# Kernel tuning notes

Hardware: AMD Instinct MI355X
Metric: run time of the kernel (lower is better)

## Reference

```python
import jax, jax.numpy as jnp
import numpy as np

D = 1024
H = 16
HD = D // H


def setup_inputs() -> dict:
    key = jax.random.key(0)
    k1, k2, k3 = jax.random.split(key, 3)
    x = jax.random.normal(k1, (4, 2048, D), dtype=jnp.float32)
    # torch Linear weight is [out, in]; we store transposed [in, out] for x @ W
    w_qkv = jax.random.normal(k2, (D, 3 * D), dtype=jnp.float32) * (1.0 / np.sqrt(D))
    w_o = jax.random.normal(k3, (D, D), dtype=jnp.float32) * (1.0 / np.sqrt(D))
    return {"x": x, "w_qkv": w_qkv, "w_o": w_o}


def reference(x, w_qkv, w_o):
    B, T, _ = x.shape
    qkv = x @ w_qkv                                  # [B, T, 3D]
    q, k, v = jnp.split(qkv, 3, axis=-1)
    def heads(t):
        return t.reshape(B, T, H, HD).transpose(0, 2, 1, 3)  # [B, H, T, hd]
    q, k, v = heads(q), heads(k), heads(v)
    scale = 1.0 / jnp.sqrt(jnp.asarray(HD, x.dtype))
    att = jnp.einsum("bhtd,bhsd->bhts", q, k) * scale       # [B, H, T, T]
    att = jax.nn.softmax(att, axis=-1)
    y = jnp.einsum("bhts,bhsd->bhtd", att, v)                # [B, H, T, hd]
    y = y.transpose(0, 2, 1, 3).reshape(B, T, D)
    return y @ w_o
```

## Files before the change

### kernel.cpp

```cpp
#include <hip/hip_runtime.h>
#include <hip/hip_bf16.h>
#include <stdint.h>

typedef __attribute__((ext_vector_type(8))) short short8;
typedef __attribute__((ext_vector_type(4))) float f32x4;

#define MFMA_BF16(a, b, c) __builtin_amdgcn_mfma_f32_16x16x32_bf16((a), (b), (c), 0, 0, 0)

#define QSCALE 0.18033688011118293f

__device__ __forceinline__ unsigned short f2bf(float f) {
  unsigned int u = __builtin_bit_cast(unsigned int, f);
  u += 0x7fffu + ((u >> 16) & 1u);
  return (unsigned short)(u >> 16);
}

__device__ __forceinline__ uint32_t pkbf(float a, float b) {
  float2 f; f.x = a; f.y = b;
  __hip_bfloat162 h = __float22bfloat162_rn(f);
  uint32_t u;
  __builtin_memcpy(&u, &h, 4);
  return u;
}

__device__ __forceinline__ float exp2_fast(float x) {
#if __has_builtin(__builtin_amdgcn_exp2f)
  return __builtin_amdgcn_exp2f(x);
#else
  float r;
  asm("v_exp_f32 %0, %1" : "=v"(r) : "v"(x));
  return r;
#endif
}

__device__ __forceinline__ void gload_lds16(const void* g, void* l) {
  __builtin_amdgcn_global_load_lds(
      (const __attribute__((address_space(1))) unsigned int*)g,
      (__attribute__((address_space(3))) unsigned int*)l, 16, 0, 0);
}

__global__ __launch_bounds__(256) void cvt_f32_bf16_k(const float* __restrict__ in,
                                                      unsigned short* __restrict__ out,
                                                      int n8) {
  int i = blockIdx.x * 256 + threadIdx.x;
  if (i >= n8) return;
  const float4* p = (const float4*)(in + (size_t)i * 8);
  float4 a = p[0], b = p[1];
  short8 o;
  o[0] = (short)f2bf(a.x); o[1] = (short)f2bf(a.y);
  o[2] = (short)f2bf(a.z); o[3] = (short)f2bf(a.w);
  o[4] = (short)f2bf(b.x); o[5] = (short)f2bf(b.y);
  o[6] = (short)f2bf(b.z); o[7] = (short)f2bf(b.w);
  *(short8*)(out + (size_t)i * 8) = o;
}

__global__ __launch_bounds__(256) void transpose_f32_bf16_k(const float* __restrict__ in,
                                                            unsigned short* __restrict__ out,
                                                            int R, int C) {
  __shared__ __attribute__((aligned(16))) unsigned short t[64][65];
  int c0 = blockIdx.x * 64, r0 = blockIdx.y * 64;
  int tx = threadIdx.x;
  for (int rr = threadIdx.y; rr < 64; rr += 4)
    t[rr][tx] = f2bf(in[(size_t)(r0 + rr) * C + c0 + tx]);
  __syncthreads();
  for (int rr = threadIdx.y; rr < 64; rr += 4)
    out[(size_t)(c0 + rr) * R + r0 + tx] = t[tx][rr];
}

template <int MODE, int NT>
__global__ __launch_bounds__(256, 3) void gemm_bt_k(
    const unsigned short* __restrict__ A, const unsigned short* __restrict__ Bt,
    float* __restrict__ Cout, unsigned short* __restrict__ Qd,
    unsigned short* __restrict__ Kd, unsigned short* __restrict__ Vtd,
    int M, int N, int Kdim) {
  __shared__ __attribute__((aligned(16))) unsigned short As[3][4096];
  __shared__ __attribute__((aligned(16))) unsigned short Bs[3][4096];
  const int tid = threadIdx.x, lane = tid & 63, w = tid >> 6;
  const int wr = w >> 1, wc = w & 1;
  const int lo = lane & 15, hi = lane >> 4;
  const int nwg = gridDim.x;
  const int newid = (blockIdx.x & 7) * (nwg >> 3) + (blockIdx.x >> 3);
  const int tn = newid % NT, tm = newid / NT;
  f32x4 acc[4][4] = {};
  const char* Ab = (const char*)A;
  const char* Bb = (const char*)Bt;
  const int nk = Kdim >> 5;

#define GSTAGE(kt, bb)                                                        \
  {                                                                           \
    _Pragma("unroll") for (int j = 0; j < 2; ++j) {                           \
      int o8 = w * 2048 + j * 1024 + lane * 16;                               \
      int src = o8 ^ (((o8 >> 6) & 3) << 4);                                  \
      int row = src >> 6, cb = src & 63;                                      \
      gload_lds16(Ab + ((size_t)(tm * 128 + row) * Kdim + (kt) * 32) * 2 + cb,\
                  (char*)As[bb] + o8);                                        \
      gload_lds16(Bb + ((size_t)(tn * 128 + row) * Kdim + (kt) * 32) * 2 + cb,\
                  (char*)Bs[bb] + o8);                                        \
    }                                                                         \
  }

  GSTAGE(0, 0);
  GSTAGE(1, 1);
  asm volatile("s_waitcnt vmcnt(4)" ::: "memory");
  __builtin_amdgcn_s_barrier();
  int gbuf = 0;
  for (int kt = 0; kt < nk; ++kt) {
    if (kt + 2 < nk) {
      int nb = gbuf + 2; if (nb >= 3) nb -= 3;
      GSTAGE(kt + 2, nb);
    }
    short8 af[4], bf[4];
#pragma unroll
    for (int m = 0; m < 4; ++m) {
      int r = wr * 64 + m * 16 + lo;
      int ad = (r * 64 + hi * 16) ^ ((r & 3) << 4);
      af[m] = *(const short8*)((const char*)As[gbuf] + ad);
    }
#pragma unroll
    for (int n = 0; n < 4; ++n) {
      int r = wc * 64 + n * 16 + lo;
      int ad = (r * 64 + hi * 16) ^ ((r & 3) << 4);
      bf[n] = *(const short8*)((const char*)Bs[gbuf] + ad);
    }
    __builtin_amdgcn_s_setprio(1);
#pragma unroll
    for (int m = 0; m < 4; ++m)
#pragma unroll
      for (int n = 0; n < 4; ++n)
        acc[m][n] = MFMA_BF16(af[m], bf[n], acc[m][n]);
    __builtin_amdgcn_s_setprio(0);
    if (kt + 2 < nk)
      asm volatile("s_waitcnt vmcnt(4)" ::: "memory");
    else
      asm volatile("s_waitcnt vmcnt(0)" ::: "memory");
    __builtin_amdgcn_s_barrier();
    gbuf = (gbuf + 1 == 3) ? 0 : gbuf + 1;
  }
  if (MODE == 1) {
#pragma unroll
    for (int m = 0; m < 4; ++m)
#pragma unroll
      for (int n = 0; n < 4; ++n)
#pragma unroll
        for (int j = 0; j < 4; ++j) {
          int row = tm * 128 + wr * 64 + m * 16 + hi * 4 + j;
          int col = tn * 128 + wc * 64 + n * 16 + lo;
          Cout[(size_t)row * N + col] = acc[m][n][j];
        }
  } else {
    int which = (tn * 128) >> 10;
#pragma unroll
    for (int m = 0; m < 4; ++m)
#pragma unroll
      for (int n = 0; n < 4; ++n)
#pragma unroll
        for (int j = 0; j < 4; ++j) {
          int row = tm * 128 + wr * 64 + m * 16 + hi * 4 + j;
          int col = tn * 128 + wc * 64 + n * 16 + lo;
          int b = row >> 11, t = row & 2047;
          int rem = col & 1023;
          int h = rem >> 6, hd = rem & 63;
          float v = acc[m][n][j];
          if (which == 0)
            Qd[((size_t)(b * 16 + h) * 2048 + t) * 64 + hd] = f2bf(v * QSCALE);
          else if (which == 1)
            Kd[((size_t)(b * 16 + h) * 2048 + t) * 64 + hd] = f2bf(v);
          else
            Vtd[((size_t)(b * 16 + h) * 64 + hd) * 2048 + t] = f2bf(v);
        }
  }
}

__global__ __launch_bounds__(512) void attn_k(const unsigned short* __restrict__ Qd,
                                              const unsigned short* __restrict__ Kd,
                                              const unsigned short* __restrict__ Vtd,
                                              unsigned short* __restrict__ Y) {
  const int T = 2048, NT = 32;
  int flat = blockIdx.x;
  int qt = (flat >> 3) & 7;
  int bh = (flat & 7) * 8 + (flat >> 6);
  int tid = threadIdx.x, lane = tid & 63, w = tid >> 6;
  int lo = lane & 15, hi = lane >> 4;
  const unsigned short* Qbh = Qd + (size_t)bh * T * 64;
  const char* Kb = (const char*)(Kd + (size_t)bh * T * 64);
  const char* Vb = (const char*)(Vtd + (size_t)bh * 64 * T);

  __shared__ __attribute__((aligned(16))) unsigned short Ks[3][4096];
  __shared__ __attribute__((aligned(16))) unsigned short Vs[3][4096];
  __shared__ __attribute__((aligned(16))) unsigned short Ps[8][2][1024];

  const short8 ones = {0x3F80, 0x3F80, 0x3F80, 0x3F80,
                       0x3F80, 0x3F80, 0x3F80, 0x3F80};

  short8 qf[2][2];
#pragma unroll
  for (int qh = 0; qh < 2; ++qh) {
    const unsigned short* qrow =
        Qbh + (size_t)(qt * 256 + w * 32 + qh * 16 + lo) * 64 + hi * 8;
    qf[qh][0] = *(const short8*)qrow;
    qf[qh][1] = *(const short8*)(qrow + 32);
  }
  f32x4 oacc[2][4] = {};
  f32x4 lacc[2] = {};

#define STAGE(kt, b)                                                          \
  {                                                                           \
    int base = w * 1024;                                                      \
    int o8 = base + lane * 16;                                                \
    int src = o8 ^ (((o8 >> 7) & 7) << 4);                                    \
    gload_lds16(Kb + (size_t)(kt) * 8192 + src, (char*)Ks[b] + base);         \
    int hd_ = src >> 7, cbyt = src & 127;                                     \
    gload_lds16(Vb + (size_t)hd_ * (T * 2) + (size_t)(kt) * 128 + cbyt,       \
                (char*)Vs[b] + base);                                         \
  }

  STAGE(0, 0);
  STAGE(1, 1);
  asm volatile("s_waitcnt vmcnt(2)" ::: "memory");
  __builtin_amdgcn_s_barrier();
  int bufc = 0;
  for (int kt = 0; kt < NT; ++kt) {
    if (kt + 2 < NT) {
      int nb = bufc + 2; if (nb >= 3) nb -= 3;
      STAGE(kt + 2, nb);
    }

    f32x4 sacc[2][4] = {};
    __builtin_amdgcn_s_setprio(1);
#pragma unroll
    for (int st = 0; st < 4; ++st)
#pragma unroll
      for (int c = 0; c < 2; ++c) {
        int row = st * 16 + lo;
        int addr = (row * 128 + c * 64 + hi * 16) ^ ((row & 7) << 4);
        short8 kf = *(const short8*)((const char*)Ks[bufc] + addr);
        sacc[0][st] = MFMA_BF16(kf, qf[0][c], sacc[0][st]);
        sacc[1][st] = MFMA_BF16(kf, qf[1][c], sacc[1][st]);
      }
    __builtin_amdgcn_s_setprio(0);

#pragma unroll
    for (int qh = 0; qh < 2; ++qh) {
      char* pw = (char*)&Ps[w][qh][0];
#pragma unroll
      for (int st = 0; st < 4; ++st) {
        float p0 = exp2_fast(sacc[qh][st][0]);
        float p1 = exp2_fast(sacc[qh][st][1]);
        float p2 = exp2_fast(sacc[qh][st][2]);
        float p3 = exp2_fast(sacc[qh][st][3]);
        int wb = (lo * 128 + st * 32 + hi * 8) ^ ((lo & 7) << 4);
        *(uint32_t*)(pw + wb) = pkbf(p0, p1);
        *(uint32_t*)(pw + wb + 4) = pkbf(p2, p3);
      }
    }

    __builtin_amdgcn_s_setprio(1);
#pragma unroll
    for (int c = 0; c < 2; ++c) {
      int pb = (lo * 128 + c * 64 + hi * 16) ^ ((lo & 7) << 4);
      short8 pf0 = *(const short8*)((const char*)&Ps[w][0][0] + pb);
      short8 pf1 = *(const short8*)((const char*)&Ps[w][1][0] + pb);
      lacc[0] = MFMA_BF16(pf0, ones, lacc[0]);
      lacc[1] = MFMA_BF16(pf1, ones, lacc[1]);
#pragma unroll
      for (int n = 0; n < 4; ++n) {
        int row = n * 16 + lo;
        int addr = (row * 128 + c * 64 + hi * 16) ^ ((row & 7) << 4);
        short8 vf = *(const short8*)((const char*)Vs[bufc] + addr);
        oacc[0][n] = MFMA_BF16(pf0, vf, oacc[0][n]);
        oacc[1][n] = MFMA_BF16(pf1, vf, oacc[1][n]);
      }
    }
    __builtin_amdgcn_s_setprio(0);

    if (kt + 2 < NT)
      asm volatile("s_waitcnt vmcnt(2)" ::: "memory");
    else
      asm volatile("s_waitcnt vmcnt(0)" ::: "memory");
    __builtin_amdgcn_s_barrier();
    bufc = (bufc + 1 == 3) ? 0 : bufc + 1;
  }

  int b = bh >> 4, h = bh & 15;
#pragma unroll
  for (int qh = 0; qh < 2; ++qh)
#pragma unroll
    for (int r = 0; r < 4; ++r) {
      int t = qt * 256 + w * 32 + qh * 16 + hi * 4 + r;
      float rl = 1.0f / lacc[qh][r];
#pragma unroll
      for (int n = 0; n < 4; ++n) {
        int hd = n * 16 + lo;
        Y[((size_t)(b * 2048 + t)) * 1024 + h * 64 + hd] =
            f2bf(oacc[qh][n][r] * rl);
      }
    }
}

extern "C" void kernel_launch(void* const* d_in, const int* in_sizes, int n_in,
                              void* d_out, int out_size, void* d_ws, size_t ws_size,
                              hipStream_t stream) {
  const float* x = (const float*)d_in[0];
  const float* w_qkv = (const float*)d_in[1];
  const float* w_o = (const float*)d_in[2];
  float* out = (float*)d_out;
  char* ws = (char*)d_ws;
  unsigned short* xb    = (unsigned short*)(ws + 0);
  unsigned short* wqkvT = (unsigned short*)(ws + 16777216);
  unsigned short* woT   = (unsigned short*)(ws + 23068672);
  unsigned short* qb    = (unsigned short*)(ws + 25165824);
  unsigned short* kb    = (unsigned short*)(ws + 41943040);
  unsigned short* vtb   = (unsigned short*)(ws + 58720256);
  unsigned short* yb    = xb;

  cvt_f32_bf16_k<<<4096, 256, 0, stream>>>(x, xb, 1048576);
  transpose_f32_bf16_k<<<dim3(48, 16), dim3(64, 4), 0, stream>>>(w_qkv, wqkvT, 1024, 3072);
  transpose_f32_bf16_k<<<dim3(16, 16), dim3(64, 4), 0, stream>>>(w_o, woT, 1024, 1024);
  gemm_bt_k<0, 24><<<1536, 256, 0, stream>>>(xb, wqkvT, nullptr, qb, kb, vtb,
                                             8192, 3072, 1024);
  attn_k<<<512, 512, 0, stream>>>(qb, kb, vtb, yb);
  gemm_bt_k<1, 8><<<512, 256, 0, stream>>>(yb, woT, out, nullptr, nullptr, nullptr,
                                           8192, 1024, 1024);
}
```

Measured before the change: 215.7 us.

## Give each attention wave 64 query rows with 256-thread blocks

```diff
diff --git a/kernel.cpp b/kernel.cpp
--- a/kernel.cpp
+++ b/kernel.cpp
@@ -171,7 +171,7 @@
   }
 }
 
-__global__ __launch_bounds__(512) void attn_k(const unsigned short* __restrict__ Qd,
+__global__ __launch_bounds__(256) void attn_k(const unsigned short* __restrict__ Qd,
                                               const unsigned short* __restrict__ Kd,
                                               const unsigned short* __restrict__ Vtd,
                                               unsigned short* __restrict__ Y) {
@@ -187,36 +187,38 @@
 
   __shared__ __attribute__((aligned(16))) unsigned short Ks[3][4096];
   __shared__ __attribute__((aligned(16))) unsigned short Vs[3][4096];
-  __shared__ __attribute__((aligned(16))) unsigned short Ps[8][2][1024];
+  __shared__ __attribute__((aligned(16))) unsigned short Ps[4][4][1024];
 
   const short8 ones = {0x3F80, 0x3F80, 0x3F80, 0x3F80,
                        0x3F80, 0x3F80, 0x3F80, 0x3F80};
 
-  short8 qf[2][2];
-#pragma unroll
-  for (int qh = 0; qh < 2; ++qh) {
+  short8 qf[4][2];
+#pragma unroll
+  for (int qh = 0; qh < 4; ++qh) {
     const unsigned short* qrow =
-        Qbh + (size_t)(qt * 256 + w * 32 + qh * 16 + lo) * 64 + hi * 8;
+        Qbh + (size_t)(qt * 256 + w * 64 + qh * 16 + lo) * 64 + hi * 8;
     qf[qh][0] = *(const short8*)qrow;
     qf[qh][1] = *(const short8*)(qrow + 32);
   }
-  f32x4 oacc[2][4] = {};
-  f32x4 lacc[2] = {};
+  f32x4 oacc[4][4] = {};
+  f32x4 lacc[4] = {};
 
 #define STAGE(kt, b)                                                          \
   {                                                                           \
-    int base = w * 1024;                                                      \
-    int o8 = base + lane * 16;                                                \
-    int src = o8 ^ (((o8 >> 7) & 7) << 4);                                    \
-    gload_lds16(Kb + (size_t)(kt) * 8192 + src, (char*)Ks[b] + base);         \
-    int hd_ = src >> 7, cbyt = src & 127;                                     \
-    gload_lds16(Vb + (size_t)hd_ * (T * 2) + (size_t)(kt) * 128 + cbyt,       \
-                (char*)Vs[b] + base);                                         \
+    _Pragma("unroll") for (int j = 0; j < 2; ++j) {                           \
+      int dst = w * 2048 + j * 1024;                                          \
+      int o8 = dst + lane * 16;                                               \
+      int src = o8 ^ (((o8 >> 7) & 7) << 4);                                  \
+      gload_lds16(Kb + (size_t)(kt) * 8192 + src, (char*)Ks[b] + dst);        \
+      int hd_ = src >> 7, cbyt = src & 127;                                   \
+      gload_lds16(Vb + (size_t)hd_ * (T * 2) + (size_t)(kt) * 128 + cbyt,     \
+                  (char*)Vs[b] + dst);                                        \
+    }                                                                         \
   }
 
   STAGE(0, 0);
   STAGE(1, 1);
-  asm volatile("s_waitcnt vmcnt(2)" ::: "memory");
+  asm volatile("s_waitcnt vmcnt(4)" ::: "memory");
   __builtin_amdgcn_s_barrier();
   int bufc = 0;
   for (int kt = 0; kt < NT; ++kt) {
@@ -225,7 +227,7 @@
       STAGE(kt + 2, nb);
     }
 
-    f32x4 sacc[2][4] = {};
+    f32x4 sacc[4][4] = {};
     __builtin_amdgcn_s_setprio(1);
 #pragma unroll
     for (int st = 0; st < 4; ++st)
@@ -234,13 +236,14 @@
         int row = st * 16 + lo;
         int addr = (row * 128 + c * 64 + hi * 16) ^ ((row & 7) << 4);
         short8 kf = *(const short8*)((const char*)Ks[bufc] + addr);
-        sacc[0][st] = MFMA_BF16(kf, qf[0][c], sacc[0][st]);
-        sacc[1][st] = MFMA_BF16(kf, qf[1][c], sacc[1][st]);
+#pragma unroll
+        for (int qh = 0; qh < 4; ++qh)
+          sacc[qh][st] = MFMA_BF16(kf, qf[qh][c], sacc[qh][st]);
       }
     __builtin_amdgcn_s_setprio(0);
 
 #pragma unroll
-    for (int qh = 0; qh < 2; ++qh) {
+    for (int qh = 0; qh < 4; ++qh) {
       char* pw = (char*)&Ps[w][qh][0];
 #pragma unroll
       for (int st = 0; st < 4; ++st) {
@@ -249,8 +252,10 @@
         float p2 = exp2_fast(sacc[qh][st][2]);
         float p3 = exp2_fast(sacc[qh][st][3]);
         int wb = (lo * 128 + st * 32 + hi * 8) ^ ((lo & 7) << 4);
-        *(uint32_t*)(pw + wb) = pkbf(p0, p1);
-        *(uint32_t*)(pw + wb + 4) = pkbf(p2, p3);
+        uint2 pk;
+        pk.x = pkbf(p0, p1);
+        pk.y = pkbf(p2, p3);
+        *(uint2*)(pw + wb) = pk;
       }
     }
 
@@ -258,23 +263,26 @@
 #pragma unroll
     for (int c = 0; c < 2; ++c) {
       int pb = (lo * 128 + c * 64 + hi * 16) ^ ((lo & 7) << 4);
-      short8 pf0 = *(const short8*)((const char*)&Ps[w][0][0] + pb);
-      short8 pf1 = *(const short8*)((const char*)&Ps[w][1][0] + pb);
-      lacc[0] = MFMA_BF16(pf0, ones, lacc[0]);
-      lacc[1] = MFMA_BF16(pf1, ones, lacc[1]);
+      short8 pf[4];
+#pragma unroll
+      for (int qh = 0; qh < 4; ++qh) {
+        pf[qh] = *(const short8*)((const char*)&Ps[w][qh][0] + pb);
+        lacc[qh] = MFMA_BF16(pf[qh], ones, lacc[qh]);
+      }
 #pragma unroll
       for (int n = 0; n < 4; ++n) {
         int row = n * 16 + lo;
         int addr = (row * 128 + c * 64 + hi * 16) ^ ((row & 7) << 4);
         short8 vf = *(const short8*)((const char*)Vs[bufc] + addr);
-        oacc[0][n] = MFMA_BF16(pf0, vf, oacc[0][n]);
-        oacc[1][n] = MFMA_BF16(pf1, vf, oacc[1][n]);
+#pragma unroll
+        for (int qh = 0; qh < 4; ++qh)
+          oacc[qh][n] = MFMA_BF16(pf[qh], vf, oacc[qh][n]);
       }
     }
     __builtin_amdgcn_s_setprio(0);
 
     if (kt + 2 < NT)
-      asm volatile("s_waitcnt vmcnt(2)" ::: "memory");
+      asm volatile("s_waitcnt vmcnt(4)" ::: "memory");
     else
       asm volatile("s_waitcnt vmcnt(0)" ::: "memory");
     __builtin_amdgcn_s_barrier();
@@ -283,10 +291,10 @@
 
   int b = bh >> 4, h = bh & 15;
 #pragma unroll
-  for (int qh = 0; qh < 2; ++qh)
+  for (int qh = 0; qh < 4; ++qh)
 #pragma unroll
     for (int r = 0; r < 4; ++r) {
-      int t = qt * 256 + w * 32 + qh * 16 + hi * 4 + r;
+      int t = qt * 256 + w * 64 + qh * 16 + hi * 4 + r;
       float rl = 1.0f / lacc[qh][r];
 #pragma unroll
       for (int n = 0; n < 4; ++n) {
@@ -318,7 +326,7 @@
   transpose_f32_bf16_k<<<dim3(16, 16), dim3(64, 4), 0, stream>>>(w_o, woT, 1024, 1024);
   gemm_bt_k<0, 24><<<1536, 256, 0, stream>>>(xb, wqkvT, nullptr, qb, kb, vtb,
                                              8192, 3072, 1024);
-  attn_k<<<512, 512, 0, stream>>>(qb, kb, vtb, yb);
+  attn_k<<<512, 256, 0, stream>>>(qb, kb, vtb, yb);
   gemm_bt_k<1, 8><<<512, 256, 0, stream>>>(yb, woT, out, nullptr, nullptr, nullptr,
                                            8192, 1024, 1024);
 }
```

New measurement: 262.4 us. 21.7% more time.
